# Kernel tuning notes

Measured on AMD Instinct MI355X. Metric: run time of the kernel, lower is better.

Reference implementation:

```python
import jax, jax.numpy as jnp
import numpy as np

D_MODEL = 1024
D_STATE = 16
D_CONV = 4
EXPAND = 2
D_INNER = D_MODEL * EXPAND
BATCH = 4
SEQ_LEN = 4096


def setup_inputs() -> dict:
    key = jax.random.key(0)
    ks = jax.random.split(key, 6)
    def rn(k, shape, scale):
        return jax.random.normal(k, shape, dtype=jnp.float32) * scale
    x = rn(ks[0], (BATCH, SEQ_LEN, D_MODEL), 1.0)
    in_proj_w = rn(ks[1], (2 * D_INNER, D_MODEL), D_MODEL ** -0.5)
    conv_w = rn(ks[2], (D_INNER, 1, D_CONV), D_CONV ** -0.5)  # depthwise conv kernel
    conv_b = rn(ks[3], (D_INNER,), 0.02)
    x_proj_w = rn(ks[4], (2 * D_STATE + 1, D_INNER), D_INNER ** -0.5)
    A_log = jnp.log(jnp.arange(1, D_STATE + 1, dtype=jnp.float32))  # module's init
    D = jnp.ones((D_INNER,), jnp.float32)
    out_proj_w = rn(ks[5], (D_MODEL, D_INNER), D_INNER ** -0.5)
    return dict(x=x, in_proj_w=in_proj_w, conv_w=conv_w, conv_b=conv_b,
                x_proj_w=x_proj_w, A_log=A_log, D=D, out_proj_w=out_proj_w)


def _silu(v):
    return v * jax.nn.sigmoid(v)


def reference(x, in_proj_w, conv_w, conv_b, x_proj_w, A_log, D, out_proj_w):
    b, l, _ = x.shape
    # input projection -> (b, l, 2*d_inner), split into x_inner and gate z
    xz = jnp.einsum('bld,ed->ble', x, in_proj_w)
    x_inner, z = jnp.split(xz, 2, axis=-1)
    # causal depthwise conv1d: torch pads both sides d_conv-1 then truncates to l,
    # equivalent to left-pad d_conv-1 only
    xc = jnp.transpose(x_inner, (0, 2, 1))  # (b, d_inner, l)
    xc = jax.lax.conv_general_dilated(
        xc, conv_w, window_strides=(1,), padding=[(D_CONV - 1, 0)],
        feature_group_count=D_INNER, dimension_numbers=('NCH', 'OIH', 'NCH'))
    xc = xc + conv_b[None, :, None]
    x_conv = _silu(jnp.transpose(xc, (0, 2, 1)))  # (b, l, d_inner)
    # SSM parameter projection: [delta(1) | B(d_state) | C(d_state)]
    x_dbl = jnp.einsum('bld,ed->ble', x_conv, x_proj_w)
    delta = jax.nn.softplus(x_dbl[..., 0])       # (b, l) scalar per token
    B_ssm = x_dbl[..., 1:D_STATE + 1]            # (b, l, n)
    C_ssm = x_dbl[..., D_STATE + 1:]             # (b, l, n)
    A = -jnp.exp(A_log)                          # (n,)

    def step(h, inp):
        x_t, d_t, B_t, C_t = inp  # (b,d_inner), (b,), (b,n), (b,n)
        dA = jnp.exp(d_t[:, None, None] * A)          # (b, 1, n)
        dB = d_t[:, None, None] * B_t[:, None, :]     # (b, 1, n)
        h = h * dA + x_t[:, :, None] * dB             # (b, d_inner, n)
        y_t = jnp.einsum('bdn,bn->bd', h, C_t)
        return h, y_t

    h0 = jnp.zeros((b, D_INNER, D_STATE), x.dtype)
    xs = (jnp.swapaxes(x_conv, 0, 1), jnp.swapaxes(delta, 0, 1),
          jnp.swapaxes(B_ssm, 0, 1), jnp.swapaxes(C_ssm, 0, 1))
    _, ys = jax.lax.scan(step, h0, xs)  # ys: (l, b, d_inner)
    y = jnp.swapaxes(ys, 0, 1)
    y = y + x_conv * D
    y = y * _silu(z)
    return jnp.einsum('bld,od->blo', y, out_proj_w)
```

## Files before the change

### kernel.cpp

```cpp
#include <hip/hip_runtime.h>
#include <hip/hip_fp16.h>

typedef _Float16 f16;
typedef _Float16 half8 __attribute__((ext_vector_type(8)));
typedef _Float16 half4v __attribute__((ext_vector_type(4)));
typedef float f32x4 __attribute__((ext_vector_type(4)));

#define AS1(p) ((const __attribute__((address_space(1))) void*)(p))
#define AS3(p) ((__attribute__((address_space(3))) void*)(p))

__device__ __forceinline__ void gload_lds16(const void* g, void* l) {
    __builtin_amdgcn_global_load_lds(AS1(g), AS3(l), 16, 0, 0);
}

__global__ __launch_bounds__(256) void cvt_f16_k(const float* __restrict__ in,
                                                 f16* __restrict__ out, int n4) {
    for (int i = blockIdx.x * 256 + threadIdx.x; i < n4; i += gridDim.x * 256) {
        float4 v = ((const float4*)in)[i];
        half4v o;
        o[0] = (f16)v.x; o[1] = (f16)v.y; o[2] = (f16)v.z; o[3] = (f16)v.w;
        ((half4v*)out)[i] = o;
    }
}

__global__ __launch_bounds__(256)
void wxp_cvt_k(const float* __restrict__ W, f16* __restrict__ Wh) {
    int idx = blockIdx.x * 256 + threadIdx.x;
    int e = idx >> 11;
    int k = idx & 2047;
    Wh[idx] = (e < 33) ? (f16)W[e * 2048 + k] : (f16)0.f;
}

__device__ __forceinline__ void stage_q(const f16* __restrict__ g, int ld,
                                        int row0, int gk, f16* q,
                                        int tid, int wave) {
#pragma unroll
    for (int rd = 0; rd < 2; ++rd) {
        int t = rd * 512 + tid;
        int r = t >> 2;
        int cu = (t & 3) ^ ((r >> 1) & 3);
        gload_lds16(g + (size_t)(row0 + r) * ld + gk + cu * 8,
                    q + rd * 4096 + wave * 512);
    }
}

#define PH(Q, KH, MH, LOADB, STAGE, WAITC)                                    \
  {                                                                           \
    half8 afr[4];                                                             \
    {                                                                         \
      const f16* aq = &lds[Q][0][KH][0];                                      \
      int ra = wm * 128 + (MH) * 64 + lr;                                     \
      afr[0] = *(const half8*)(aq + (ra +  0) * 32 + cofs);                   \
      afr[1] = *(const half8*)(aq + (ra + 16) * 32 + cofs);                   \
      afr[2] = *(const half8*)(aq + (ra + 32) * 32 + cofs);                   \
      afr[3] = *(const half8*)(aq + (ra + 48) * 32 + cofs);                   \
    }                                                                         \
    if (LOADB) {                                                              \
      const f16* bq = &lds[Q][1][KH][0];                                      \
      int rb = wn * 64 + lr;                                                  \
      bfr[0] = *(const half8*)(bq + (rb +  0) * 32 + cofs);                   \
      bfr[1] = *(const half8*)(bq + (rb + 16) * 32 + cofs);                   \
      bfr[2] = *(const half8*)(bq + (rb + 32) * 32 + cofs);                   \
      bfr[3] = *(const half8*)(bq + (rb + 48) * 32 + cofs);                   \
    }                                                                         \
    STAGE;                                                                    \
    __builtin_amdgcn_s_barrier();                                             \
    asm volatile("s_waitcnt lgkmcnt(0)" ::: "memory");                        \
    __builtin_amdgcn_sched_barrier(0);                                        \
    __builtin_amdgcn_s_setprio(1);                                            \
    _Pragma("unroll")                                                         \
    for (int f_ = 0; f_ < 4; ++f_)                                            \
      _Pragma("unroll")                                                       \
      for (int j_ = 0; j_ < 4; ++j_)                                          \
        acc[(MH) * 4 + f_][j_] = __builtin_amdgcn_mfma_f32_16x16x32_f16(      \
            afr[f_], bfr[j_], acc[(MH) * 4 + f_][j_], 0, 0, 0);               \
    __builtin_amdgcn_s_setprio(0);                                            \
    __builtin_amdgcn_sched_barrier(0);                                        \
    WAITC;                                                                    \
    __builtin_amdgcn_s_barrier();                                             \
  }

template <typename OutT>
__global__ __launch_bounds__(512, 2)
void gemm8p(const f16* __restrict__ A, const f16* __restrict__ B,
            OutT* __restrict__ C, int N, int K, int lda, int ldc) {
    __shared__ f16 lds[2][2][2][8192];

    int nTn = N >> 8;
    unsigned bid = blockIdx.x;
    unsigned cpx = gridDim.x >> 3;
    bid = (bid & 7u) * cpx + (bid >> 3);
    int bm = (int)(bid / nTn) * 256;
    int bn = (int)(bid % nTn) * 256;

    int tid = threadIdx.x;
    int wave = tid >> 6;
    int lane = tid & 63;
    int wm = wave >> 2;
    int wn = wave & 3;
    int lr = lane & 15;
    int cg = lane >> 4;
    int cofs = ((cg ^ ((lr >> 1) & 3)) << 3);

    f32x4 acc[8][4];
#pragma unroll
    for (int i = 0; i < 8; ++i)
#pragma unroll
        for (int j = 0; j < 4; ++j) acc[i][j] = (f32x4){0.f, 0.f, 0.f, 0.f};
    half8 bfr[4];

    stage_q(B, K,   bn, 0,  &lds[0][1][0][0], tid, wave);
    stage_q(A, lda, bm, 0,  &lds[0][0][0][0], tid, wave);
    stage_q(B, K,   bn, 32, &lds[0][1][1][0], tid, wave);
    stage_q(A, lda, bm, 32, &lds[0][0][1][0], tid, wave);
    stage_q(B, K,   bn, 64, &lds[1][1][0][0], tid, wave);
    stage_q(A, lda, bm, 64, &lds[1][0][0][0], tid, wave);
    stage_q(B, K,   bn, 96, &lds[1][1][1][0], tid, wave);
    asm volatile("s_waitcnt vmcnt(6)" ::: "memory");
    __builtin_amdgcn_s_barrier();

    int NI = K >> 7;
    for (int it = 0; it < NI; ++it) {
        int gk = it << 7;
        bool last = (it == NI - 1);
        PH(0, 0, 0, true,
           { stage_q(A, lda, bm, gk + 96, &lds[1][0][1][0], tid, wave); }, {});
        PH(0, 0, 1, false,
           { if (!last) stage_q(B, K, bn, gk + 128, &lds[0][1][0][0], tid, wave); }, {});
        PH(0, 1, 0, true,
           { if (!last) stage_q(A, lda, bm, gk + 128, &lds[0][0][0][0], tid, wave); }, {});
        PH(0, 1, 1, false,
           { if (!last) stage_q(B, K, bn, gk + 160, &lds[0][1][1][0], tid, wave); },
           { if (last) asm volatile("s_waitcnt vmcnt(0)" ::: "memory");
             else      asm volatile("s_waitcnt vmcnt(6)" ::: "memory"); });
        PH(1, 0, 0, true,
           { if (!last) stage_q(A, lda, bm, gk + 160, &lds[0][0][1][0], tid, wave); }, {});
        PH(1, 0, 1, false,
           { if (!last) stage_q(B, K, bn, gk + 192, &lds[1][1][0][0], tid, wave); }, {});
        PH(1, 1, 0, true,
           { if (!last) stage_q(A, lda, bm, gk + 192, &lds[1][0][0][0], tid, wave); }, {});
        PH(1, 1, 1, false,
           { if (!last) stage_q(B, K, bn, gk + 224, &lds[1][1][1][0], tid, wave); },
           { if (!last) asm volatile("s_waitcnt vmcnt(6)" ::: "memory"); });
    }

    int orow0 = bm + wm * 128 + (lane >> 4) * 4;
    int ocol0 = bn + wn * 64 + lr;
#pragma unroll
    for (int mf = 0; mf < 8; ++mf)
#pragma unroll
        for (int nj = 0; nj < 4; ++nj)
#pragma unroll
            for (int r = 0; r < 4; ++r)
                C[(size_t)(orow0 + mf * 16 + r) * ldc + (ocol0 + nj * 16)] =
                    (OutT)acc[mf][nj][r];
}

__global__ __launch_bounds__(256, 2)
void xdbl_mfma_k(const f16* __restrict__ xc, const f16* __restrict__ Wh,
                 float* __restrict__ xdbl) {
    __shared__ f16 As[64 * 64];
    __shared__ f16 Bs[48 * 64];
    int bm = blockIdx.x * 64;
    int tid = threadIdx.x;
    int wave = tid >> 6;
    int lane = tid & 63;
    int srow = lane >> 3;
    int scol = (lane & 7) * 8;
    int lr = lane & 15;
    int lkh = (lane >> 4) * 8;

    f32x4 acc[3];
#pragma unroll
    for (int j = 0; j < 3; ++j) acc[j] = (f32x4){0.f, 0.f, 0.f, 0.f};

    for (int k0 = 0; k0 < 2048; k0 += 64) {
        __syncthreads();
#pragma unroll
        for (int i = 0; i < 2; ++i) {
            int slot = wave * 2 + i;
            gload_lds16(xc + (size_t)(bm + slot * 8 + srow) * 2048 + (k0 + scol),
                        As + slot * 512);
        }
        if (wave < 3) {
#pragma unroll
            for (int i = 0; i < 2; ++i) {
                int slot = wave * 2 + i;
                gload_lds16(Wh + (size_t)(slot * 8 + srow) * 2048 + (k0 + scol),
                            Bs + slot * 512);
            }
        }
        asm volatile("s_waitcnt vmcnt(0)" ::: "memory");
        __syncthreads();
#pragma unroll
        for (int kk = 0; kk < 2; ++kk) {
            half8 a = *(const half8*)(As + (wave * 16 + lr) * 64 + kk * 32 + lkh);
#pragma unroll
            for (int nj = 0; nj < 3; ++nj) {
                half8 b = *(const half8*)(Bs + (nj * 16 + lr) * 64 + kk * 32 + lkh);
                acc[nj] = __builtin_amdgcn_mfma_f32_16x16x32_f16(a, b, acc[nj], 0, 0, 0);
            }
        }
    }

    int orow0 = bm + wave * 16 + (lane >> 4) * 4;
#pragma unroll
    for (int nj = 0; nj < 3; ++nj) {
        int col = nj * 16 + lr;
        if (col < 33) {
#pragma unroll
            for (int r = 0; r < 4; ++r)
                xdbl[(size_t)(orow0 + r) * 33 + col] = acc[nj][r];
        }
    }
}

__global__ __launch_bounds__(256)
void conv_silu_k(const f16* __restrict__ xz, const float* __restrict__ cw,
                 const float* __restrict__ cb, f16* __restrict__ xc) {
    int r0 = blockIdx.x * 8;
    int d0 = threadIdx.x << 3;
    int l0 = r0 & 4095;

    const float4* cw4 = (const float4*)cw;
    float4 w[8];
    float bias[8];
#pragma unroll
    for (int e = 0; e < 8; ++e) { w[e] = cw4[d0 + e]; bias[e] = cb[d0 + e]; }

    half8 xv[11];
#pragma unroll
    for (int j = 0; j < 11; ++j) {
        if (l0 - 3 + j >= 0)
            xv[j] = *(const half8*)(xz + (size_t)(r0 - 3 + j) * 4096 + d0);
        else
            xv[j] = (half8){};
    }

#pragma unroll
    for (int rr = 0; rr < 8; ++rr) {
        float acc[8];
#pragma unroll
        for (int e = 0; e < 8; ++e) acc[e] = bias[e];
#pragma unroll
        for (int k = 0; k < 4; ++k) {
            half8 xk = xv[rr + k];
#pragma unroll
            for (int e = 0; e < 8; ++e) {
                float wj = (k == 0) ? w[e].x : (k == 1) ? w[e].y : (k == 2) ? w[e].z : w[e].w;
                acc[e] = fmaf((float)xk[e], wj, acc[e]);
            }
        }
        half8 out = {};
#pragma unroll
        for (int e = 0; e < 8; ++e) {
            float v = acc[e];
            out[e] = (f16)(v / (1.f + expf(-v)));
        }
        *(half8*)(xc + (size_t)(r0 + rr) * 2048 + d0) = out;
    }
}

__global__ __launch_bounds__(256)
void sp_build_k(const float* __restrict__ xdbl, const float* __restrict__ A_log,
                float* __restrict__ SP, float* __restrict__ dlt) {
    int m = blockIdx.x * 256 + threadIdx.x;
    const float* row = xdbl + (size_t)m * 33;
    float v0 = row[0];
    float d = (v0 > 15.f) ? v0 : logf(1.f + expf(v0));
    dlt[m] = d;
    float* sp = SP + (size_t)m * 48;
#pragma unroll
    for (int n = 0; n < 16; ++n) {
        float An = -expf(A_log[n]);
        sp[n] = expf(An * d);
        sp[16 + n] = d * row[1 + n];
        sp[32 + n] = row[17 + n];
    }
}

__global__ __launch_bounds__(128)
void g_build_k(const float* __restrict__ dlt, const float* __restrict__ A_log,
               float* __restrict__ G) {
    __shared__ float red[128];
    int bc = blockIdx.x, t = threadIdx.x;
    red[t] = dlt[bc * 128 + t];
    __syncthreads();
#pragma unroll
    for (int s = 64; s > 0; s >>= 1) {
        if (t < s) red[t] += red[t + s];
        __syncthreads();
    }
    if (t < 16) G[bc * 16 + t] = expf(-expf(A_log[t]) * red[0]);
}

__global__ __launch_bounds__(256)
void scan1_k(const f16* __restrict__ xc, const float* __restrict__ SP,
             float* __restrict__ F) {
    __shared__ float sp[128 * 48];
    int blk = blockIdx.x;
    int dg = blk & 7;
    int bc = blk >> 3;
    int tid = threadIdx.x;
    int wave = tid >> 6;
    int d = dg * 256 + tid;
    int mbase = bc * 128;

    const char* spb = (const char*)(SP + (size_t)mbase * 48);
#pragma unroll
    for (int i = 0; i < 6; ++i)
        gload_lds16(spb + (size_t)(i * 256 + tid) * 16,
                    (char*)sp + (size_t)(i * 256 + wave * 64) * 16);
    asm volatile("s_waitcnt vmcnt(0)" ::: "memory");
    __syncthreads();

    float h[16];
#pragma unroll
    for (int n = 0; n < 16; ++n) h[n] = 0.f;

#pragma unroll 2
    for (int tt = 0; tt < 128; ++tt) {
        const float* r = sp + tt * 48;
        float x = (float)xc[(size_t)(mbase + tt) * 2048 + d];
#pragma unroll
        for (int n = 0; n < 16; ++n) h[n] = fmaf(h[n], r[n], x * r[16 + n]);
    }
    size_t fb = ((size_t)bc * 2048 + d) * 16;
#pragma unroll
    for (int n = 0; n < 16; ++n) F[fb + n] = h[n];
}

__global__ __launch_bounds__(256)
void combine_k(const float* __restrict__ F, const float* __restrict__ G,
               float* __restrict__ H0) {
    int gid = blockIdx.x * 256 + threadIdx.x;
    int b = gid >> 11;
    int d = gid & 2047;
    float h[16];
#pragma unroll
    for (int n = 0; n < 16; ++n) h[n] = 0.f;
    for (int c = 0; c < 32; ++c) {
        int bc = b * 32 + c;
        size_t base = ((size_t)bc * 2048 + d) * 16;
#pragma unroll
        for (int n = 0; n < 16; ++n) H0[base + n] = h[n];
#pragma unroll
        for (int n = 0; n < 16; ++n) h[n] = fmaf(G[bc * 16 + n], h[n], F[base + n]);
    }
}

__global__ __launch_bounds__(256)
void scan2_k(const f16* __restrict__ xc, const f16* xz, const float* __restrict__ SP,
             const float* __restrict__ H0, const float* __restrict__ Dv,
             f16* yout) {
    __shared__ float sp[128 * 48];
    int blk = blockIdx.x;
    int dg = blk & 7;
    int bc = blk >> 3;
    int tid = threadIdx.x;
    int wave = tid >> 6;
    int d = dg * 256 + tid;
    int mbase = bc * 128;

    const char* spb = (const char*)(SP + (size_t)mbase * 48);
#pragma unroll
    for (int i = 0; i < 6; ++i)
        gload_lds16(spb + (size_t)(i * 256 + tid) * 16,
                    (char*)sp + (size_t)(i * 256 + wave * 64) * 16);
    asm volatile("s_waitcnt vmcnt(0)" ::: "memory");
    __syncthreads();

    size_t fb = ((size_t)bc * 2048 + d) * 16;
    float h[16];
#pragma unroll
    for (int n = 0; n < 16; ++n) h[n] = H0[fb + n];
    float Dd = Dv[d];

#pragma unroll 2
    for (int tt = 0; tt < 128; ++tt) {
        const float* r = sp + tt * 48;
        size_t mrow = (size_t)(mbase + tt);
        float x = (float)xc[mrow * 2048 + d];
        float z = (float)xz[mrow * 4096 + 2048 + d];
        float y0 = 0.f, y1 = 0.f, y2 = 0.f, y3 = 0.f;
#pragma unroll
        for (int n = 0; n < 16; n += 4) {
            h[n]     = fmaf(h[n],     r[n],     x * r[16 + n]);
            h[n + 1] = fmaf(h[n + 1], r[n + 1], x * r[17 + n]);
            h[n + 2] = fmaf(h[n + 2], r[n + 2], x * r[18 + n]);
            h[n + 3] = fmaf(h[n + 3], r[n + 3], x * r[19 + n]);
            y0 = fmaf(h[n],     r[32 + n], y0);
            y1 = fmaf(h[n + 1], r[33 + n], y1);
            y2 = fmaf(h[n + 2], r[34 + n], y2);
            y3 = fmaf(h[n + 3], r[35 + n], y3);
        }
        float y = (y0 + y1) + (y2 + y3);
        float yf = fmaf(x, Dd, y);
        float sz = z / (1.f + expf(-z));
        yout[mrow * 4096 + d] = (f16)(yf * sz);
    }
}

extern "C" void kernel_launch(void* const* d_in, const int* in_sizes, int n_in,
                              void* d_out, int out_size, void* d_ws, size_t ws_size,
                              hipStream_t stream) {
    const float* x      = (const float*)d_in[0];
    const float* w_in   = (const float*)d_in[1];
    const float* conv_w = (const float*)d_in[2];
    const float* conv_b = (const float*)d_in[3];
    const float* w_xp   = (const float*)d_in[4];
    const float* A_log  = (const float*)d_in[5];
    const float* Dv     = (const float*)d_in[6];
    const float* w_out  = (const float*)d_in[7];

    char* base = (char*)d_ws;
    f16* xzh = (f16*)base;
    char* r1 = base + 134217728;
    f16* xh  = (f16*)r1;
    f16* wih = (f16*)(r1 + 33554432);
    f16* xch = (f16*)r1;
    f16* woh = (f16*)r1;
    char* p = base + 201326592;
    float* xdbl = (float*)p;  p += 2162688;
    float* dlt  = (float*)p;  p += 65536;
    float* SP   = (float*)p;  p += 3145728;
    float* G    = (float*)p;  p += 8192;
    float* F    = (float*)p;  p += 16777216;
    float* H0   = (float*)p;  p += 16777216;
    f16*   Wh   = (f16*)p;    p += 196608;

    cvt_f16_k<<<2048, 256, 0, stream>>>(x, xh, 4194304);
    cvt_f16_k<<<2048, 256, 0, stream>>>(w_in, wih, 1048576);
    wxp_cvt_k<<<384, 256, 0, stream>>>(w_xp, Wh);

    gemm8p<f16><<<1024, 512, 0, stream>>>(xh, wih, xzh, 4096, 1024, 1024, 4096);

    conv_silu_k<<<2048, 256, 0, stream>>>(xzh, conv_w, conv_b, xch);

    xdbl_mfma_k<<<256, 256, 0, stream>>>(xch, Wh, xdbl);

    sp_build_k<<<64, 256, 0, stream>>>(xdbl, A_log, SP, dlt);
    g_build_k<<<128, 128, 0, stream>>>(dlt, A_log, G);

    scan1_k<<<1024, 256, 0, stream>>>(xch, SP, F);
    combine_k<<<32, 256, 0, stream>>>(F, G, H0);
    scan2_k<<<1024, 256, 0, stream>>>(xch, xzh, SP, H0, Dv, xzh);

    cvt_f16_k<<<2048, 256, 0, stream>>>(w_out, woh, 524288);

    gemm8p<float><<<256, 512, 0, stream>>>(xzh, woh, (float*)d_out,
                                           1024, 2048, 4096, 1024);
}
```

Baseline: 483.6 us.

## Fuse prep conversions, persistent in_proj GEMM, merge SP/G build, parallelize combine

Merges the three fp32-to-fp16 conversion kernels into one launch, and merges the SP build and G reduction into a single kernel. The in_proj GEMM becomes persistent: 256 blocks each process 4 tiles, prefetching the next tile's first K-slices during the last iteration of the current one. combine_k now uses one thread per (b,d,n) element with 512 blocks instead of 32, which exposes far more parallelism and gives coalesced access. The changes trim launch overhead and GEMM tile-transition gaps and fix an under-parallelized combine, at the cost of more complex pipeline control in the GEMM.

```diff
diff --git a/kernel.cpp b/kernel.cpp
--- a/kernel.cpp
+++ b/kernel.cpp
@@ -11,6 +11,31 @@
 
 __device__ __forceinline__ void gload_lds16(const void* g, void* l) {
     __builtin_amdgcn_global_load_lds(AS1(g), AS3(l), 16, 0, 0);
+}
+
+__global__ __launch_bounds__(256)
+void prep_k(const float* __restrict__ x, const float* __restrict__ w_in,
+            const float* __restrict__ w_xp,
+            f16* __restrict__ xh, f16* __restrict__ wih, f16* __restrict__ Wh) {
+    int b = blockIdx.x;
+    if (b < 2048) {
+        for (int i = b * 256 + threadIdx.x; i < 4194304; i += 2048 * 256) {
+            float4 v = ((const float4*)x)[i];
+            half4v o; o[0] = (f16)v.x; o[1] = (f16)v.y; o[2] = (f16)v.z; o[3] = (f16)v.w;
+            ((half4v*)xh)[i] = o;
+        }
+    } else if (b < 2560) {
+        for (int i = (b - 2048) * 256 + threadIdx.x; i < 1048576; i += 512 * 256) {
+            float4 v = ((const float4*)w_in)[i];
+            half4v o; o[0] = (f16)v.x; o[1] = (f16)v.y; o[2] = (f16)v.z; o[3] = (f16)v.w;
+            ((half4v*)wih)[i] = o;
+        }
+    } else {
+        int idx = (b - 2560) * 256 + threadIdx.x;
+        int e = idx >> 11;
+        int k = idx & 2047;
+        Wh[idx] = (e < 33) ? (f16)w_xp[e * 2048 + k] : (f16)0.f;
+    }
 }
 
 __global__ __launch_bounds__(256) void cvt_f16_k(const float* __restrict__ in,
@@ -21,14 +46,6 @@
         o[0] = (f16)v.x; o[1] = (f16)v.y; o[2] = (f16)v.z; o[3] = (f16)v.w;
         ((half4v*)out)[i] = o;
     }
-}
-
-__global__ __launch_bounds__(256)
-void wxp_cvt_k(const float* __restrict__ W, f16* __restrict__ Wh) {
-    int idx = blockIdx.x * 256 + threadIdx.x;
-    int e = idx >> 11;
-    int k = idx & 2047;
-    Wh[idx] = (e < 33) ? (f16)W[e * 2048 + k] : (f16)0.f;
 }
 
 __device__ __forceinline__ void stage_q(const f16* __restrict__ g, int ld,
@@ -80,18 +97,15 @@
     __builtin_amdgcn_s_barrier();                                             \
   }
 
-template <typename OutT>
+template <typename OutT, int NT>
 __global__ __launch_bounds__(512, 2)
-void gemm8p(const f16* __restrict__ A, const f16* __restrict__ B,
-            OutT* __restrict__ C, int N, int K, int lda, int ldc) {
+void gemm8p_pers(const f16* __restrict__ A, const f16* __restrict__ B,
+                 OutT* __restrict__ C, int N, int K, int lda, int ldc) {
     __shared__ f16 lds[2][2][2][8192];
 
     int nTn = N >> 8;
-    unsigned bid = blockIdx.x;
-    unsigned cpx = gridDim.x >> 3;
-    bid = (bid & 7u) * cpx + (bid >> 3);
-    int bm = (int)(bid / nTn) * 256;
-    int bn = (int)(bid % nTn) * 256;
+    unsigned grid = gridDim.x;
+    unsigned cpx = (grid * (unsigned)NT) >> 3;
 
     int tid = threadIdx.x;
     int wave = tid >> 6;
@@ -108,6 +122,16 @@
 #pragma unroll
         for (int j = 0; j < 4; ++j) acc[i][j] = (f32x4){0.f, 0.f, 0.f, 0.f};
     half8 bfr[4];
+
+    auto tileMN = [&](int j, int& tm, int& tn) {
+        unsigned o = blockIdx.x + grid * (unsigned)j;
+        unsigned s = (o & 7u) * cpx + (o >> 3);
+        tm = (int)(s / (unsigned)nTn) * 256;
+        tn = (int)(s % (unsigned)nTn) * 256;
+    };
+
+    int bm, bn;
+    tileMN(0, bm, bn);
 
     stage_q(B, K,   bn, 0,  &lds[0][1][0][0], tid, wave);
     stage_q(A, lda, bm, 0,  &lds[0][0][0][0], tid, wave);
@@ -120,40 +144,55 @@
     __builtin_amdgcn_s_barrier();
 
     int NI = K >> 7;
-    for (int it = 0; it < NI; ++it) {
-        int gk = it << 7;
-        bool last = (it == NI - 1);
-        PH(0, 0, 0, true,
-           { stage_q(A, lda, bm, gk + 96, &lds[1][0][1][0], tid, wave); }, {});
-        PH(0, 0, 1, false,
-           { if (!last) stage_q(B, K, bn, gk + 128, &lds[0][1][0][0], tid, wave); }, {});
-        PH(0, 1, 0, true,
-           { if (!last) stage_q(A, lda, bm, gk + 128, &lds[0][0][0][0], tid, wave); }, {});
-        PH(0, 1, 1, false,
-           { if (!last) stage_q(B, K, bn, gk + 160, &lds[0][1][1][0], tid, wave); },
-           { if (last) asm volatile("s_waitcnt vmcnt(0)" ::: "memory");
-             else      asm volatile("s_waitcnt vmcnt(6)" ::: "memory"); });
-        PH(1, 0, 0, true,
-           { if (!last) stage_q(A, lda, bm, gk + 160, &lds[0][0][1][0], tid, wave); }, {});
-        PH(1, 0, 1, false,
-           { if (!last) stage_q(B, K, bn, gk + 192, &lds[1][1][0][0], tid, wave); }, {});
-        PH(1, 1, 0, true,
-           { if (!last) stage_q(A, lda, bm, gk + 192, &lds[1][0][0][0], tid, wave); }, {});
-        PH(1, 1, 1, false,
-           { if (!last) stage_q(B, K, bn, gk + 224, &lds[1][1][1][0], tid, wave); },
-           { if (!last) asm volatile("s_waitcnt vmcnt(6)" ::: "memory"); });
-    }
-
-    int orow0 = bm + wm * 128 + (lane >> 4) * 4;
-    int ocol0 = bn + wn * 64 + lr;
-#pragma unroll
-    for (int mf = 0; mf < 8; ++mf)
-#pragma unroll
-        for (int nj = 0; nj < 4; ++nj)
-#pragma unroll
-            for (int r = 0; r < 4; ++r)
-                C[(size_t)(orow0 + mf * 16 + r) * ldc + (ocol0 + nj * 16)] =
-                    (OutT)acc[mf][nj][r];
+    for (int j = 0; j < NT; ++j) {
+        int bm2 = bm, bn2 = bn;
+        if (j + 1 < NT) tileMN(j + 1, bm2, bn2);
+
+        for (int it = 0; it < NI; ++it) {
+            int gk = it << 7;
+            bool lastIter = (it == NI - 1);
+            bool fin = lastIter && (j + 1 == NT);
+            int sbm = lastIter ? bm2 : bm;
+            int sbn = lastIter ? bn2 : bn;
+            int sgk = lastIter ? 0 : gk + 128;
+
+            PH(0, 0, 0, true,
+               { stage_q(A, lda, bm, gk + 96, &lds[1][0][1][0], tid, wave); }, {});
+            PH(0, 0, 1, false,
+               { if (!fin) stage_q(B, K, sbn, sgk, &lds[0][1][0][0], tid, wave); }, {});
+            PH(0, 1, 0, true,
+               { if (!fin) stage_q(A, lda, sbm, sgk, &lds[0][0][0][0], tid, wave); }, {});
+            PH(0, 1, 1, false,
+               { if (!fin) stage_q(B, K, sbn, sgk + 32, &lds[0][1][1][0], tid, wave); },
+               { if (fin) asm volatile("s_waitcnt vmcnt(0)" ::: "memory");
+                 else     asm volatile("s_waitcnt vmcnt(6)" ::: "memory"); });
+            PH(1, 0, 0, true,
+               { if (!fin) stage_q(A, lda, sbm, sgk + 32, &lds[0][0][1][0], tid, wave); }, {});
+            PH(1, 0, 1, false,
+               { if (!fin) stage_q(B, K, sbn, sgk + 64, &lds[1][1][0][0], tid, wave); }, {});
+            PH(1, 1, 0, true,
+               { if (!fin) stage_q(A, lda, sbm, sgk + 64, &lds[1][0][0][0], tid, wave); }, {});
+            PH(1, 1, 1, false,
+               { if (!fin) stage_q(B, K, sbn, sgk + 96, &lds[1][1][1][0], tid, wave); },
+               { if (!fin) asm volatile("s_waitcnt vmcnt(6)" ::: "memory"); });
+        }
+
+        int orow0 = bm + wm * 128 + (lane >> 4) * 4;
+        int ocol0 = bn + wn * 64 + lr;
+#pragma unroll
+        for (int mf = 0; mf < 8; ++mf)
+#pragma unroll
+            for (int nj = 0; nj < 4; ++nj)
+#pragma unroll
+                for (int r = 0; r < 4; ++r)
+                    C[(size_t)(orow0 + mf * 16 + r) * ldc + (ocol0 + nj * 16)] =
+                        (OutT)acc[mf][nj][r];
+#pragma unroll
+        for (int i2 = 0; i2 < 8; ++i2)
+#pragma unroll
+            for (int j2 = 0; j2 < 4; ++j2) acc[i2][j2] = (f32x4){0.f, 0.f, 0.f, 0.f};
+        bm = bm2; bn = bn2;
+    }
 }
 
 __global__ __launch_bounds__(256, 2)
@@ -261,14 +300,16 @@
     }
 }
 
-__global__ __launch_bounds__(256)
-void sp_build_k(const float* __restrict__ xdbl, const float* __restrict__ A_log,
-                float* __restrict__ SP, float* __restrict__ dlt) {
-    int m = blockIdx.x * 256 + threadIdx.x;
+__global__ __launch_bounds__(128)
+void spg_k(const float* __restrict__ xdbl, const float* __restrict__ A_log,
+           float* __restrict__ SP, float* __restrict__ G) {
+    __shared__ float red[128];
+    int bc = blockIdx.x;
+    int t = threadIdx.x;
+    int m = bc * 128 + t;
     const float* row = xdbl + (size_t)m * 33;
     float v0 = row[0];
     float d = (v0 > 15.f) ? v0 : logf(1.f + expf(v0));
-    dlt[m] = d;
     float* sp = SP + (size_t)m * 48;
 #pragma unroll
     for (int n = 0; n < 16; ++n) {
@@ -277,14 +318,7 @@
         sp[16 + n] = d * row[1 + n];
         sp[32 + n] = row[17 + n];
     }
-}
-
-__global__ __launch_bounds__(128)
-void g_build_k(const float* __restrict__ dlt, const float* __restrict__ A_log,
-               float* __restrict__ G) {
-    __shared__ float red[128];
-    int bc = blockIdx.x, t = threadIdx.x;
-    red[t] = dlt[bc * 128 + t];
+    red[t] = d;
     __syncthreads();
 #pragma unroll
     for (int s = 64; s > 0; s >>= 1) {
@@ -334,18 +368,15 @@
 void combine_k(const float* __restrict__ F, const float* __restrict__ G,
                float* __restrict__ H0) {
     int gid = blockIdx.x * 256 + threadIdx.x;
-    int b = gid >> 11;
-    int d = gid & 2047;
-    float h[16];
-#pragma unroll
-    for (int n = 0; n < 16; ++n) h[n] = 0.f;
+    int b = gid >> 15;
+    int dn = gid & 32767;
+    int n = dn & 15;
+    float h = 0.f;
     for (int c = 0; c < 32; ++c) {
         int bc = b * 32 + c;
-        size_t base = ((size_t)bc * 2048 + d) * 16;
-#pragma unroll
-        for (int n = 0; n < 16; ++n) H0[base + n] = h[n];
-#pragma unroll
-        for (int n = 0; n < 16; ++n) h[n] = fmaf(G[bc * 16 + n], h[n], F[base + n]);
+        size_t idx = (size_t)bc * 32768 + dn;
+        H0[idx] = h;
+        h = fmaf(G[bc * 16 + n], h, F[idx]);
     }
 }
 
@@ -422,32 +453,29 @@
     f16* woh = (f16*)r1;
     char* p = base + 201326592;
     float* xdbl = (float*)p;  p += 2162688;
-    float* dlt  = (float*)p;  p += 65536;
+    p += 65536;
     float* SP   = (float*)p;  p += 3145728;
     float* G    = (float*)p;  p += 8192;
     float* F    = (float*)p;  p += 16777216;
     float* H0   = (float*)p;  p += 16777216;
     f16*   Wh   = (f16*)p;    p += 196608;
 
-    cvt_f16_k<<<2048, 256, 0, stream>>>(x, xh, 4194304);
-    cvt_f16_k<<<2048, 256, 0, stream>>>(w_in, wih, 1048576);
-    wxp_cvt_k<<<384, 256, 0, stream>>>(w_xp, Wh);
-
-    gemm8p<f16><<<1024, 512, 0, stream>>>(xh, wih, xzh, 4096, 1024, 1024, 4096);
+    prep_k<<<2944, 256, 0, stream>>>(x, w_in, w_xp, xh, wih, Wh);
+
+    gemm8p_pers<f16, 4><<<256, 512, 0, stream>>>(xh, wih, xzh, 4096, 1024, 1024, 4096);
 
     conv_silu_k<<<2048, 256, 0, stream>>>(xzh, conv_w, conv_b, xch);
 
     xdbl_mfma_k<<<256, 256, 0, stream>>>(xch, Wh, xdbl);
 
-    sp_build_k<<<64, 256, 0, stream>>>(xdbl, A_log, SP, dlt);
-    g_build_k<<<128, 128, 0, stream>>>(dlt, A_log, G);
+    spg_k<<<128, 128, 0, stream>>>(xdbl, A_log, SP, G);
 
     scan1_k<<<1024, 256, 0, stream>>>(xch, SP, F);
-    combine_k<<<32, 256, 0, stream>>>(F, G, H0);
+    combine_k<<<512, 256, 0, stream>>>(F, G, H0);
     scan2_k<<<1024, 256, 0, stream>>>(xch, xzh, SP, H0, Dv, xzh);
 
     cvt_f16_k<<<2048, 256, 0, stream>>>(w_out, woh, 524288);
 
-    gemm8p<float><<<256, 512, 0, stream>>>(xzh, woh, (float*)d_out,
-                                           1024, 2048, 4096, 1024);
-}
+    gemm8p_pers<float, 1><<<256, 512, 0, stream>>>(xzh, woh, (float*)d_out,
+                                                   1024, 2048, 4096, 1024);
+}
```

New measurement: 446.1 us. 7.7% less time.
